# Kernel tuning notes

Hardware: AMD Instinct MI355X
Metric: run time of the kernel (lower is better)

Reference implementation:

```python
import jax, jax.numpy as jnp
import numpy as np

N = 8192
IN_F = 128
OUT_F = 128
ALPHA = 0.2  # LeakyReLU negative slope
NEG_INF = -9e15


def setup_inputs() -> dict:
    key = jax.random.key(0)
    k1, k2, k3, k4, k5 = jax.random.split(key, 5)
    mole_out = jax.random.normal(k1, (N, IN_F), dtype=jnp.float32)
    adj = jax.random.randint(k2, (N, N), 0, 2, dtype=jnp.int32)
    # nn.Linear(in_features, out_features, bias=False): y = x @ W  (W stored as [in, out])
    W = jax.random.normal(k3, (IN_F, OUT_F), dtype=jnp.float32) / np.sqrt(IN_F)
    # nn.Linear(2*out_features, 1, bias=False) weight split into a1 (for Wh_i) and a2 (for Wh_j)
    a1 = jax.random.normal(k4, (OUT_F,), dtype=jnp.float32) / np.sqrt(2 * OUT_F)
    a2 = jax.random.normal(k5, (OUT_F,), dtype=jnp.float32) / np.sqrt(2 * OUT_F)
    return {"mole_out": mole_out, "adj": adj, "W": W, "a1": a1, "a2": a2}


def reference(mole_out, adj, W, a1, a2):
    Wh = mole_out @ W                       # (N, F)
    # a([Wh_i || Wh_j]) = a1.Wh_i + a2.Wh_j  -- avoids the O(N^2*2F) concat tensor
    s1 = Wh @ a1                            # (N,)
    s2 = Wh @ a2                            # (N,)
    e = jax.nn.leaky_relu(s1[:, None] + s2[None, :], negative_slope=ALPHA)  # (N, N)
    att = jnp.where(adj > 0, e, NEG_INF)
    att = jax.nn.softmax(att, axis=1)       # row softmax over neighbors j
    # dropout_gnn = 0.0 -> identity
    h_prime = att @ Wh                      # (N, F)
    return jax.nn.elu(h_prime)              # concat=True branch
```

## Files before the change

### kernel.cpp

```cpp
#include <hip/hip_runtime.h>
#include <hip/hip_bf16.h>

#define NROW 8192
#define NF   128
#define LOG2E 1.4426950408889634f

typedef float f32x4  __attribute__((ext_vector_type(4)));
typedef int   i32x4  __attribute__((ext_vector_type(4)));
typedef short bf16x8 __attribute__((ext_vector_type(8)));
typedef short bf16x4 __attribute__((ext_vector_type(4)));
typedef unsigned long long u64;

__device__ __forceinline__ short f2bf(float f) {
    union { float f; unsigned u; } v; v.f = f;
    unsigned r = v.u + 0x7FFFu + ((v.u >> 16) & 1u);
    return (short)(r >> 16);
}

__device__ __forceinline__ void gload_lds16(const short* g, short* l) {
    __builtin_amdgcn_global_load_lds(
        (const __attribute__((address_space(1))) void*)g,
        (__attribute__((address_space(3))) void*)l, 16, 0, 0);
}


__global__ __launch_bounds__(256) void k0_wt(const float* __restrict__ W,
                                             short* __restrict__ WT) {
    int idx = blockIdx.x * 256 + threadIdx.x;
    int c = idx >> 7, k = idx & 127;
    WT[c * NF + k] = f2bf(W[k * NF + c]);
}

__global__ __launch_bounds__(256) void k1_wh(const float* __restrict__ mo,
        const short* __restrict__ WT,
        const float* __restrict__ a1, const float* __restrict__ a2,
        short* __restrict__ WhT, float* __restrict__ s1g, float* __restrict__ s2g) {
    __shared__ float s_lds[2][32];
    int t = threadIdx.x;
    int w = t >> 6, l = t & 63, lg = l >> 4, lr = l & 15;
    int rows0 = blockIdx.x * 32;
    if (t < 64) s_lds[t >> 5][t & 31] = 0.0f;
    __syncthreads();

    f32x4 acc[2][2] = {};
#pragma unroll
    for (int ks = 0; ks < 4; ++ks) {
        bf16x8 a[2], b[2];
#pragma unroll
        for (int rt = 0; rt < 2; ++rt) {
            const float* ap = mo + (size_t)(rows0 + rt*16 + lr) * NF + ks*32 + lg*8;
            f32x4 x0 = *(const f32x4*)ap;
            f32x4 x1 = *(const f32x4*)(ap + 4);
#pragma unroll
            for (int e = 0; e < 4; ++e) { a[rt][e] = f2bf(x0[e]); a[rt][4+e] = f2bf(x1[e]); }
        }
#pragma unroll
        for (int ct = 0; ct < 2; ++ct) {
            int c = w*32 + ct*16 + lr;
            b[ct] = *(const bf16x8*)(WT + c*NF + ks*32 + lg*8);
        }
#pragma unroll
        for (int rt = 0; rt < 2; ++rt)
#pragma unroll
            for (int ct = 0; ct < 2; ++ct)
                acc[rt][ct] = __builtin_amdgcn_mfma_f32_16x16x32_bf16(a[rt], b[ct], acc[rt][ct], 0, 0, 0);
    }

#pragma unroll
    for (int rt = 0; rt < 2; ++rt) {
        float p1[4] = {0,0,0,0}, p2[4] = {0,0,0,0};
#pragma unroll
        for (int ct = 0; ct < 2; ++ct) {
            int c = w*32 + ct*16 + lr;
            float a1c = a1[c], a2c = a2[c];
            bf16x4 wv;
#pragma unroll
            for (int g = 0; g < 4; ++g) {
                float v = acc[rt][ct][g];
                wv[g] = f2bf(v);
                p1[g] += v * a1c;
                p2[g] += v * a2c;
            }
            int r0 = rows0 + rt*16 + lg*4;
            size_t off = (size_t)(r0 >> 6) * 8192 + (size_t)(c >> 4) * 1024
                       + (size_t)((r0 >> 5) & 1) * 512 + (size_t)((r0 >> 3) & 3) * 128
                       + (size_t)(c & 15) * 8 + (size_t)(r0 & 7);
            *(bf16x4*)(WhT + off) = wv;
        }
#pragma unroll
        for (int off = 1; off < 16; off <<= 1) {
#pragma unroll
            for (int g = 0; g < 4; ++g) {
                p1[g] += __shfl_xor(p1[g], off);
                p2[g] += __shfl_xor(p2[g], off);
            }
        }
        if (lr == 0) {
            int rloc = rt*16 + lg*4;
#pragma unroll
            for (int g = 0; g < 4; ++g) {
                atomicAdd(&s_lds[0][rloc+g], p1[g]);
                atomicAdd(&s_lds[1][rloc+g], p2[g]);
            }
        }
    }
    __syncthreads();
    if (t < 32)       s1g[rows0 + t]        = s_lds[0][t] * LOG2E;
    else if (t < 64)  s2g[rows0 + (t - 32)] = s_lds[1][t - 32] * LOG2E;
}

__global__ __launch_bounds__(256, 4) void k2_main(
        const int* __restrict__ adj, const short* __restrict__ WhT,
        const float* __restrict__ s1g, const float* __restrict__ s2g,
        float* __restrict__ numP, float* __restrict__ zP,
        int S, int npb) {
    __shared__ __attribute__((aligned(16))) short Bl[16384];
    __shared__ __attribute__((aligned(16))) float s2l[2048];

    int t = threadIdx.x, w = t >> 6, l = t & 63;
    int lo = l & 15, hi = l >> 4;
    int b = blockIdx.x, jseg = b % S, rg = b / S;
    int wrows0 = (rg << 6) + (w << 4);
    int j0 = jseg * npb;
    int NT = npb >> 7;

    for (int i = t; i < (npb >> 2); i += 256)
        ((f32x4*)s2l)[i] = ((const f32x4*)(s2g + j0))[i];

    float s1v = s1g[wrows0 + lo];
    const int* arow = adj + (size_t)wrows0 * NROW + j0 + l;

    f32x4 acc[8] = {};
    float z = 0.0f;

    int An[32];
#pragma unroll
    for (int r = 0; r < 16; ++r) {
        An[r]      = arow[r * NROW];
        An[16 + r] = arow[r * NROW + 64];
    }
    {
        const short* gs = WhT + (size_t)(j0 >> 6) * 8192 + w*4096 + l*8;
        short* ds = &Bl[w*4096];
#pragma unroll
        for (int r8 = 0; r8 < 8; ++r8)
            gload_lds16(gs + r8*512, ds + r8*512);
    }
    __syncthreads();

    for (int it = 0; it < NT; ++it) {
        u64 bmqA = 0, bmqB = 0;
#pragma unroll
        for (int r = 0; r < 16; ++r) {
            u64 brA = __ballot(An[r] > 0);
            u64 brB = __ballot(An[16 + r] > 0);
            bmqA = (lo == r) ? brA : bmqA;
            bmqB = (lo == r) ? brB : bmqB;
        }
        int more = (it + 1 < NT);
        if (more) {
            int joff = (it + 1) << 7;
#pragma unroll
            for (int r = 0; r < 16; ++r) {
                An[r]      = arow[r * NROW + joff];
                An[16 + r] = arow[r * NROW + joff + 64];
            }
        }
#pragma unroll
        for (int ks = 0; ks < 4; ++ks) {
            u64 bq = (ks < 2) ? bmqA : bmqB;
            unsigned bits = (unsigned)(bq >> (((ks & 1) << 5) + hi * 8)) & 0xffu;
            int js = (it << 7) + ks * 32 + hi * 8;
            f32x4 sa = *(const f32x4*)(s2l + js);
            f32x4 sb = *(const f32x4*)(s2l + js + 4);
            float p[8];
#pragma unroll
            for (int e = 0; e < 4; ++e) {
                float x, pe;
                x = s1v + sa[e]; pe = exp2f(fmaxf(x, 0.2f * x));
                p[e]     = ((bits >> e) & 1) ? pe : 0.0f;        z += p[e];
                x = s1v + sb[e]; pe = exp2f(fmaxf(x, 0.2f * x));
                p[4 + e] = ((bits >> (4 + e)) & 1) ? pe : 0.0f;  z += p[4 + e];
            }
            union { bf16x8 v8; __hip_bfloat162 h2[4]; } fau;
#pragma unroll
            for (int q = 0; q < 4; ++q)
                fau.h2[q] = __float22bfloat162_rn(make_float2(p[2*q], p[2*q + 1]));
            const short* Bc = &Bl[(ks >> 1) * 8192 + (ks & 1) * 512 + l * 8];
#pragma unroll
            for (int ct = 0; ct < 8; ++ct) {
                bf16x8 bv = *(const bf16x8*)(Bc + ct * 1024);
                acc[ct] = __builtin_amdgcn_mfma_f32_16x16x32_bf16(fau.v8, bv, acc[ct], 0, 0, 0);
            }
        }
        __syncthreads();
        if (more) {
            const short* gs = WhT + (size_t)((j0 + ((it + 1) << 7)) >> 6) * 8192 + w*4096 + l*8;
            short* ds = &Bl[w*4096];
#pragma unroll
            for (int r8 = 0; r8 < 8; ++r8)
                gload_lds16(gs + r8*512, ds + r8*512);
            __syncthreads();
        }
    }

    z += __shfl_xor(z, 16);
    z += __shfl_xor(z, 32);
    if (l < 16) zP[(size_t)jseg * NROW + wrows0 + lo] = z;

    size_t obase = (size_t)jseg * NROW * NF;
#pragma unroll
    for (int ct = 0; ct < 8; ++ct) {
        int cc = ct * 16 + lo;
        int r0 = wrows0 + hi * 4;
#pragma unroll
        for (int g = 0; g < 4; ++g)
            numP[obase + (size_t)(r0 + g) * NF + cc] = acc[ct][g];
    }
}

__global__ __launch_bounds__(256) void k3_reduce(const float* __restrict__ numP,
        const float* __restrict__ zP, float* __restrict__ out, int S) {
    int idx = (blockIdx.x * 256 + threadIdx.x) * 4;
    int r = idx >> 7;
    f32x4 num = {};
    float zz = 0.0f;
    for (int s = 0; s < S; ++s) {
        f32x4 v = *(const f32x4*)(numP + (size_t)s * (NROW * NF) + idx);
        num += v;
        zz  += zP[s * NROW + r];
    }
    f32x4 o;
#pragma unroll
    for (int e = 0; e < 4; ++e) {
        float h = num[e] / zz;
        o[e] = (h > 0.0f) ? h : expm1f(h);
    }
    *(f32x4*)(out + idx) = o;
}

extern "C" void kernel_launch(void* const* d_in, const int* in_sizes, int n_in,
                              void* d_out, int out_size, void* d_ws, size_t ws_size,
                              hipStream_t stream) {
    const float* mo  = (const float*)d_in[0];
    const int*   adj = (const int*)d_in[1];
    const float* W   = (const float*)d_in[2];
    const float* a1  = (const float*)d_in[3];
    const float* a2  = (const float*)d_in[4];
    float* out = (float*)d_out;

    char* p = (char*)d_ws;
    short* WT  = (short*)p;  p += (size_t)NF * NF * 2;
    short* WhT = (short*)p;  p += (size_t)NF * NROW * 2;
    float* s1  = (float*)p;  p += (size_t)NROW * 4;
    float* s2  = (float*)p;  p += (size_t)NROW * 4;
    float* zP  = (float*)p;  p += (size_t)8 * NROW * 4;
    size_t fixed = (size_t)(p - (char*)d_ws);

    int S = 8;
    while (S > 1 && fixed + (size_t)S * NROW * NF * 4 > ws_size) S >>= 1;
    float* numP = (float*)p;
    if (fixed + (size_t)S * NROW * NF * 4 > ws_size) numP = out;

    k0_wt<<<dim3(64), dim3(256), 0, stream>>>(W, WT);
    k1_wh<<<dim3(256), dim3(256), 0, stream>>>(mo, WT, a1, a2, WhT, s1, s2);
    k2_main<<<dim3((NROW / 64) * S), dim3(256), 0, stream>>>(adj, WhT, s1, s2, numP, zP, S, NROW / S);
    k3_reduce<<<dim3(NROW * NF / 1024), dim3(256), 0, stream>>>(numP, zP, out, S);
}
```

Before: 88.14 us.

## Double-buffer WhT tiles in LDS with 512-thread blocks and 64-column steps

The main attention kernel moves from 256-thread blocks covering 64 rows to 512-thread blocks covering 128 rows, so each WhT tile staged in LDS is shared by twice as many warps. The column step drops from 128 to 64 and the WhT tile is double-buffered, with the next tile's global-to-LDS load issued before the current tile's MFMAs. This removes the second barrier per iteration and overlaps the copy with compute. Adjacency prefetch is interleaved with the ballots, which cuts live registers from 32 adj values to 16. The cost is twice as many loop iterations, each still ending in a block-wide barrier, and larger blocks that may lower occupancy.

```diff
diff --git a/kernel.cpp b/kernel.cpp
--- a/kernel.cpp
+++ b/kernel.cpp
@@ -109,22 +109,22 @@
     else if (t < 64)  s2g[rows0 + (t - 32)] = s_lds[1][t - 32] * LOG2E;
 }
 
-__global__ __launch_bounds__(256, 4) void k2_main(
+__global__ __launch_bounds__(512, 4) void k2_main(
         const int* __restrict__ adj, const short* __restrict__ WhT,
         const float* __restrict__ s1g, const float* __restrict__ s2g,
         float* __restrict__ numP, float* __restrict__ zP,
         int S, int npb) {
-    __shared__ __attribute__((aligned(16))) short Bl[16384];
-    __shared__ __attribute__((aligned(16))) float s2l[2048];
+    __shared__ __attribute__((aligned(16))) short Bl[2][8192];
+    __shared__ __attribute__((aligned(16))) float s2l[1024];
 
     int t = threadIdx.x, w = t >> 6, l = t & 63;
     int lo = l & 15, hi = l >> 4;
     int b = blockIdx.x, jseg = b % S, rg = b / S;
-    int wrows0 = (rg << 6) + (w << 4);
+    int wrows0 = (rg << 7) + (w << 4);
     int j0 = jseg * npb;
-    int NT = npb >> 7;
-
-    for (int i = t; i < (npb >> 2); i += 256)
+    int NT = npb >> 6;
+
+    for (int i = t; i < (npb >> 2); i += 512)
         ((f32x4*)s2l)[i] = ((const f32x4*)(s2g + j0))[i];
 
     float s1v = s1g[wrows0 + lo];
@@ -133,44 +133,37 @@
     f32x4 acc[8] = {};
     float z = 0.0f;
 
-    int An[32];
-#pragma unroll
-    for (int r = 0; r < 16; ++r) {
-        An[r]      = arow[r * NROW];
-        An[16 + r] = arow[r * NROW + 64];
-    }
+    int An[16];
+#pragma unroll
+    for (int r = 0; r < 16; ++r) An[r] = arow[r * NROW];
     {
-        const short* gs = WhT + (size_t)(j0 >> 6) * 8192 + w*4096 + l*8;
-        short* ds = &Bl[w*4096];
-#pragma unroll
-        for (int r8 = 0; r8 < 8; ++r8)
-            gload_lds16(gs + r8*512, ds + r8*512);
+        const short* gs = WhT + (size_t)(j0 >> 6) * 8192 + w*1024 + l*8;
+        short* ds = &Bl[0][w*1024];
+        gload_lds16(gs, ds);
+        gload_lds16(gs + 512, ds + 512);
     }
     __syncthreads();
 
+    int cur = 0;
     for (int it = 0; it < NT; ++it) {
-        u64 bmqA = 0, bmqB = 0;
+        u64 bmq = 0;
+        int more = (it + 1 < NT);
 #pragma unroll
         for (int r = 0; r < 16; ++r) {
-            u64 brA = __ballot(An[r] > 0);
-            u64 brB = __ballot(An[16 + r] > 0);
-            bmqA = (lo == r) ? brA : bmqA;
-            bmqB = (lo == r) ? brB : bmqB;
-        }
-        int more = (it + 1 < NT);
+            u64 br = __ballot(An[r] > 0);
+            if (more) An[r] = arow[r * NROW + ((it + 1) << 6)];
+            bmq = (lo == r) ? br : bmq;
+        }
         if (more) {
-            int joff = (it + 1) << 7;
-#pragma unroll
-            for (int r = 0; r < 16; ++r) {
-                An[r]      = arow[r * NROW + joff];
-                An[16 + r] = arow[r * NROW + joff + 64];
-            }
-        }
-#pragma unroll
-        for (int ks = 0; ks < 4; ++ks) {
-            u64 bq = (ks < 2) ? bmqA : bmqB;
-            unsigned bits = (unsigned)(bq >> (((ks & 1) << 5) + hi * 8)) & 0xffu;
-            int js = (it << 7) + ks * 32 + hi * 8;
+            const short* gs = WhT + (size_t)((j0 + ((it+1) << 6)) >> 6) * 8192 + w*1024 + l*8;
+            short* ds = &Bl[cur ^ 1][w*1024];
+            gload_lds16(gs, ds);
+            gload_lds16(gs + 512, ds + 512);
+        }
+#pragma unroll
+        for (int ks = 0; ks < 2; ++ks) {
+            unsigned bits = (unsigned)(bmq >> ((ks << 5) + hi * 8)) & 0xffu;
+            int js = (it << 6) + ks * 32 + hi * 8;
             f32x4 sa = *(const f32x4*)(s2l + js);
             f32x4 sb = *(const f32x4*)(s2l + js + 4);
             float p[8];
@@ -186,7 +179,7 @@
 #pragma unroll
             for (int q = 0; q < 4; ++q)
                 fau.h2[q] = __float22bfloat162_rn(make_float2(p[2*q], p[2*q + 1]));
-            const short* Bc = &Bl[(ks >> 1) * 8192 + (ks & 1) * 512 + l * 8];
+            const short* Bc = &Bl[cur][ks * 512 + l * 8];
 #pragma unroll
             for (int ct = 0; ct < 8; ++ct) {
                 bf16x8 bv = *(const bf16x8*)(Bc + ct * 1024);
@@ -194,14 +187,7 @@
             }
         }
         __syncthreads();
-        if (more) {
-            const short* gs = WhT + (size_t)((j0 + ((it + 1) << 7)) >> 6) * 8192 + w*4096 + l*8;
-            short* ds = &Bl[w*4096];
-#pragma unroll
-            for (int r8 = 0; r8 < 8; ++r8)
-                gload_lds16(gs + r8*512, ds + r8*512);
-            __syncthreads();
-        }
+        cur ^= 1;
     }
 
     z += __shfl_xor(z, 16);
@@ -264,6 +250,6 @@
 
     k0_wt<<<dim3(64), dim3(256), 0, stream>>>(W, WT);
     k1_wh<<<dim3(256), dim3(256), 0, stream>>>(mo, WT, a1, a2, WhT, s1, s2);
-    k2_main<<<dim3((NROW / 64) * S), dim3(256), 0, stream>>>(adj, WhT, s1, s2, numP, zP, S, NROW / S);
+    k2_main<<<dim3((NROW / 128) * S), dim3(512), 0, stream>>>(adj, WhT, s1, s2, numP, zP, S, NROW / S);
     k3_reduce<<<dim3(NROW * NF / 1024), dim3(256), 0, stream>>>(numP, zP, out, S);
 }
```

After: 99.68 us. +13.1%, slower.

## Permute column order so adjacency loads become 8-byte vector loads

Applied to the files above, without the earlier changes.

Each lane now loads two adjacent adj columns as one i32x2 instead of two scalar loads 64 columns apart. To keep the ballot bitmasks consistent, the column index j is remapped (even columns in the first half, odd in the second) when k1 writes WhT and s2. This halves the number of adjacency load instructions in the bandwidth-bound main loop. The cost is scalar bf16 stores in k1 instead of bf16x4 stores. The s2l LDS buffer is also shrunk.

```diff
diff --git a/kernel.cpp b/kernel.cpp
--- a/kernel.cpp
+++ b/kernel.cpp
@@ -7,6 +7,7 @@
 
 typedef float f32x4  __attribute__((ext_vector_type(4)));
 typedef int   i32x4  __attribute__((ext_vector_type(4)));
+typedef int   i32x2  __attribute__((ext_vector_type(2)));
 typedef short bf16x8 __attribute__((ext_vector_type(8)));
 typedef short bf16x4 __attribute__((ext_vector_type(4)));
 typedef unsigned long long u64;
@@ -15,6 +16,10 @@
     union { float f; unsigned u; } v; v.f = f;
     unsigned r = v.u + 0x7FFFu + ((v.u >> 16) & 1u);
     return (short)(r >> 16);
+}
+
+__device__ __forceinline__ int pjmap(int j) {
+    return (j & ~127) + ((j & 1) << 6) + ((j & 127) >> 1);
 }
 
 __device__ __forceinline__ void gload_lds16(const short* g, short* l) {
@@ -73,19 +78,17 @@
         for (int ct = 0; ct < 2; ++ct) {
             int c = w*32 + ct*16 + lr;
             float a1c = a1[c], a2c = a2[c];
-            bf16x4 wv;
 #pragma unroll
             for (int g = 0; g < 4; ++g) {
                 float v = acc[rt][ct][g];
-                wv[g] = f2bf(v);
                 p1[g] += v * a1c;
                 p2[g] += v * a2c;
-            }
-            int r0 = rows0 + rt*16 + lg*4;
-            size_t off = (size_t)(r0 >> 6) * 8192 + (size_t)(c >> 4) * 1024
-                       + (size_t)((r0 >> 5) & 1) * 512 + (size_t)((r0 >> 3) & 3) * 128
-                       + (size_t)(c & 15) * 8 + (size_t)(r0 & 7);
-            *(bf16x4*)(WhT + off) = wv;
+                int pj = pjmap(rows0 + rt*16 + lg*4 + g);
+                size_t off = (size_t)(pj >> 6) * 8192 + (size_t)(c >> 4) * 1024
+                           + (size_t)((pj >> 5) & 1) * 512 + (size_t)((pj >> 3) & 3) * 128
+                           + (size_t)(c & 15) * 8 + (size_t)(pj & 7);
+                WhT[off] = f2bf(v);
+            }
         }
 #pragma unroll
         for (int off = 1; off < 16; off <<= 1) {
@@ -105,8 +108,8 @@
         }
     }
     __syncthreads();
-    if (t < 32)       s1g[rows0 + t]        = s_lds[0][t] * LOG2E;
-    else if (t < 64)  s2g[rows0 + (t - 32)] = s_lds[1][t - 32] * LOG2E;
+    if (t < 32)       s1g[rows0 + t] = s_lds[0][t] * LOG2E;
+    else if (t < 64)  s2g[pjmap(rows0 + (t - 32))] = s_lds[1][t - 32] * LOG2E;
 }
 
 __global__ __launch_bounds__(256, 4) void k2_main(
@@ -115,7 +118,7 @@
         float* __restrict__ numP, float* __restrict__ zP,
         int S, int npb) {
     __shared__ __attribute__((aligned(16))) short Bl[16384];
-    __shared__ __attribute__((aligned(16))) float s2l[2048];
+    __shared__ __attribute__((aligned(16))) float s2l[1024];
 
     int t = threadIdx.x, w = t >> 6, l = t & 63;
     int lo = l & 15, hi = l >> 4;
@@ -128,17 +131,15 @@
         ((f32x4*)s2l)[i] = ((const f32x4*)(s2g + j0))[i];
 
     float s1v = s1g[wrows0 + lo];
-    const int* arow = adj + (size_t)wrows0 * NROW + j0 + l;
+    const int* arow = adj + (size_t)wrows0 * NROW + j0 + l * 2;
 
     f32x4 acc[8] = {};
     float z = 0.0f;
 
-    int An[32];
-#pragma unroll
-    for (int r = 0; r < 16; ++r) {
-        An[r]      = arow[r * NROW];
-        An[16 + r] = arow[r * NROW + 64];
-    }
+    i32x2 An[16];
+#pragma unroll
+    for (int r = 0; r < 16; ++r)
+        An[r] = *(const i32x2*)(arow + r * NROW);
     {
         const short* gs = WhT + (size_t)(j0 >> 6) * 8192 + w*4096 + l*8;
         short* ds = &Bl[w*4096];
@@ -150,21 +151,19 @@
 
     for (int it = 0; it < NT; ++it) {
         u64 bmqA = 0, bmqB = 0;
+        int more = (it + 1 < NT);
 #pragma unroll
         for (int r = 0; r < 16; ++r) {
-            u64 brA = __ballot(An[r] > 0);
-            u64 brB = __ballot(An[16 + r] > 0);
+            u64 brA = __ballot(An[r][0] > 0);
+            u64 brB = __ballot(An[r][1] > 0);
             bmqA = (lo == r) ? brA : bmqA;
             bmqB = (lo == r) ? brB : bmqB;
         }
-        int more = (it + 1 < NT);
         if (more) {
             int joff = (it + 1) << 7;
 #pragma unroll
-            for (int r = 0; r < 16; ++r) {
-                An[r]      = arow[r * NROW + joff];
-                An[16 + r] = arow[r * NROW + joff + 64];
-            }
+            for (int r = 0; r < 16; ++r)
+                An[r] = *(const i32x2*)(arow + r * NROW + joff);
         }
 #pragma unroll
         for (int ks = 0; ks < 4; ++ks) {
```

After: 90.04 us. 1.02x slower.
